# Performance work log

Hardware: AMD Instinct MI355X
Metric: run time of the kernel (lower is better)

Reference implementation:

```python
import jax, jax.numpy as jnp
import numpy as np

D_MODEL = 1024
N_HEADS = 16
HEAD_DIM = D_MODEL // N_HEADS
SEQ = 2048
BATCH = 2
ROPE_BASE = 10000.0


def rope_cos_sin(seq_len, dim, dtype=jnp.float32):
    inv_freq = 1.0 / (ROPE_BASE ** (jnp.arange(0, dim, 2, dtype=jnp.float32) / dim))
    pos = jnp.arange(seq_len, dtype=jnp.float32)
    freqs = jnp.outer(pos, inv_freq)              # [S, dim/2]
    emb = jnp.concatenate([freqs, freqs], axis=-1)  # [S, dim]
    return jnp.cos(emb).astype(dtype), jnp.sin(emb).astype(dtype)


def rotate_half(x):
    x1, x2 = jnp.split(x, 2, axis=-1)
    return jnp.concatenate([-x2, x1], axis=-1)


def setup_inputs() -> dict:
    key = jax.random.key(0)
    kx, kq, kk, kv, ko = jax.random.split(key, 5)
    x = jax.random.normal(kx, (BATCH, SEQ, D_MODEL), dtype=jnp.float32)
    # causal boolean mask, broadcastable to [B, H, S, S]
    attn_mask = jnp.tril(jnp.ones((SEQ, SEQ), dtype=bool))[None, None]
    s = 1.0 / np.sqrt(D_MODEL)
    Wq = jax.random.normal(kq, (D_MODEL, D_MODEL), dtype=jnp.float32) * s
    Wk = jax.random.normal(kk, (D_MODEL, D_MODEL), dtype=jnp.float32) * s
    Wv = jax.random.normal(kv, (D_MODEL, D_MODEL), dtype=jnp.float32) * s
    Wo = jax.random.normal(ko, (D_MODEL, D_MODEL), dtype=jnp.float32) * s
    return {"x": x, "attn_mask": attn_mask, "Wq": Wq, "Wk": Wk, "Wv": Wv, "Wo": Wo}


def reference(x, attn_mask, Wq, Wk, Wv, Wo):
    B, S, _ = x.shape
    dtype = x.dtype
    # projections (nn.Linear: x @ W.T)
    def split_heads(t):
        return t.reshape(B, S, N_HEADS, HEAD_DIM).transpose(0, 2, 1, 3)  # [B,H,S,Dh]
    q = split_heads(x @ Wq.T)
    k = split_heads(x @ Wk.T)
    v = split_heads(x @ Wv.T)
    # RoPE
    cos, sin = rope_cos_sin(S, HEAD_DIM, dtype)  # [S, Dh]
    cos = cos[None, None]
    sin = sin[None, None]
    q = q * cos + rotate_half(q) * sin
    k = k * cos + rotate_half(k) * sin
    # float mask: 0 where True, finfo.min where False
    neg = jnp.finfo(dtype).min
    float_mask = jnp.where(attn_mask, jnp.zeros((), dtype), jnp.full((), neg, dtype))
    # scaled dot product attention
    scale = 1.0 / np.sqrt(HEAD_DIM)
    scores = jnp.einsum("bhqd,bhkd->bhqk", q, k) * scale + float_mask
    attn = jax.nn.softmax(scores, axis=-1)
    out = jnp.einsum("bhqk,bhkd->bhqd", attn, v)  # [B,H,S,Dh]
    out = out.transpose(0, 2, 1, 3).reshape(B, S, D_MODEL)
    return out @ Wo.T
```

## Files before the change

### kernel.cpp

```cpp
#include <hip/hip_runtime.h>
#include <hip/hip_bf16.h>
#include <math.h>

typedef unsigned short ushort_t;
typedef __attribute__((ext_vector_type(8))) short short8;
typedef __attribute__((ext_vector_type(4))) float f32x4;

#define D_MODEL 1024
#define SEQ     2048
#define NH      16
#define HD      64
#define BATCH   2
#define M_TOTAL (BATCH * SEQ)
#define SCL     0.18033688f
#define HSZ     4194304

__device__ __forceinline__ ushort_t f2bf(float f) {
    __hip_bfloat16 h = __float2bfloat16(f);
    ushort_t u;
    __builtin_memcpy(&u, &h, 2);
    return u;
}
__device__ __forceinline__ unsigned pack2(float a, float b) {
    __hip_bfloat162 h = __float22bfloat162_rn(make_float2(a, b));
    unsigned u;
    __builtin_memcpy(&u, &h, 4);
    return u;
}
__device__ __forceinline__ float fexp2(float x) { return __builtin_amdgcn_exp2f(x); }

typedef const __attribute__((address_space(1))) void* gp_t;
typedef __attribute__((address_space(3))) void* lp_t;
__device__ __forceinline__ void cp16(const void* g, void* l) {
    __builtin_amdgcn_global_load_lds((gp_t)g, (lp_t)l, 16, 0, 0);
}

__global__ __launch_bounds__(256) void cvt_bf16(
    const float* __restrict__ x,
    const float* __restrict__ w0, const float* __restrict__ w1,
    const float* __restrict__ w2, const float* __restrict__ w3,
    ushort_t* __restrict__ xb, ushort_t* __restrict__ wb)
{
    size_t e = ((size_t)blockIdx.x * 256 + threadIdx.x) * 8;
    const float* src;
    ushort_t* dst;
    size_t off;
    if (e < (size_t)HSZ) {
        src = x; dst = xb; off = e;
    } else {
        size_t r = e - HSZ;
        int j = (int)(r >> 20);
        off = r & 1048575u;
        src = (j == 0) ? w0 : (j == 1) ? w1 : (j == 2) ? w2 : w3;
        dst = wb + ((size_t)j << 20);
    }
    float4 a = *(const float4*)&src[off];
    float4 b = *(const float4*)&src[off + 4];
    uint4 u;
    u.x = pack2(a.x, a.y);
    u.y = pack2(a.z, a.w);
    u.z = pack2(b.x, b.y);
    u.w = pack2(b.z, b.w);
    *(uint4*)&dst[off] = u;
}

__global__ __launch_bounds__(256) void rope_tab(float2* __restrict__ tab) {
    int idx = blockIdx.x * 256 + threadIdx.x;
    int i = idx & 31, s = idx >> 5;
    float invf = powf(10000.0f, -(float)(2 * i) * (1.0f / 64.0f));
    float fr = (float)s * invf;
    float sn, cs;
    sincosf(fr, &sn, &cs);
    tab[idx] = make_float2(cs, sn);
}

template <int OMODE>
__global__ __launch_bounds__(256) void gemm_k(
    const ushort_t* __restrict__ A,
    const ushort_t* __restrict__ W0, const ushort_t* __restrict__ W1,
    const ushort_t* __restrict__ W2,
    void* __restrict__ D0v, void* __restrict__ D1v, void* __restrict__ D2v,
    const float2* __restrict__ tab)
{
    __shared__ ushort_t As[128 * 32];
    __shared__ ushort_t Bs[128 * 32];
    const int K = D_MODEL;
    const int t = threadIdx.x;
    const int l = t & 63, w = t >> 6;
    const int wm = (w & 1) * 64, wn = (w >> 1) * 64;
    const int r15 = l & 15, q4 = l >> 4;
    const int m0 = blockIdx.y * 128, n0 = blockIdx.x * 128;
    const int z = blockIdx.z;
    const ushort_t* Wp = (z == 0) ? W0 : (z == 1 ? W1 : W2);
    void* Dp           = (z == 0) ? D0v : (z == 1 ? D1v : D2v);

    f32x4 acc[4][4];
#pragma unroll
    for (int i = 0; i < 4; ++i)
#pragma unroll
        for (int j = 0; j < 4; ++j) acc[i][j] = (f32x4){0.f, 0.f, 0.f, 0.f};

    for (int k0 = 0; k0 < K; k0 += 32) {
        __syncthreads();
#pragma unroll
        for (int p = 0; p < 2; ++p) {
            int idx = t + p * 256;
            int row = idx >> 2, kp = (idx & 3) * 8;
            cp16(&A [(size_t)(m0 + row) * K + k0 + kp], &As[idx * 8]);
            cp16(&Wp[(size_t)(n0 + row) * K + k0 + kp], &Bs[idx * 8]);
        }
        __syncthreads();
        short8 af[4], bfr[4];
#pragma unroll
        for (int i = 0; i < 4; ++i)
            af[i] = *(const short8*)&As[(wm + 16 * i + r15) * 32 + q4 * 8];
#pragma unroll
        for (int j = 0; j < 4; ++j)
            bfr[j] = *(const short8*)&Bs[(wn + 16 * j + r15) * 32 + q4 * 8];
#pragma unroll
        for (int i = 0; i < 4; ++i)
#pragma unroll
            for (int j = 0; j < 4; ++j)
                acc[i][j] = __builtin_amdgcn_mfma_f32_16x16x32_bf16(
                    af[i], bfr[j], acc[i][j], 0, 0, 0);
    }

    if (OMODE == 1) {
        float* Dst = (float*)Dp;
#pragma unroll
        for (int i = 0; i < 4; ++i)
#pragma unroll
            for (int j = 0; j < 4; ++j)
#pragma unroll
                for (int r = 0; r < 4; ++r) {
                    int row = m0 + wm + 16 * i + q4 * 4 + r;
                    int col = n0 + wn + 16 * j + r15;
                    Dst[(size_t)row * D_MODEL + col] = acc[i][j][r];
                }
    } else if (z < 2) {
        ushort_t* Dst = (ushort_t*)Dp;
        const float scl = (z == 0) ? SCL : 1.0f;
#pragma unroll
        for (int i = 0; i < 4; ++i) {
#pragma unroll
            for (int r = 0; r < 4; ++r) {
                int row = m0 + wm + 16 * i + q4 * 4 + r;
                int b = row >> 11, s = row & (SEQ - 1);
                const float2* trow = &tab[s * 32];
#pragma unroll
                for (int j = 0; j < 2; ++j) {
                    int col = n0 + wn + 16 * j + r15;
                    int h = col >> 6, f = 16 * j + r15;
                    float2 csn = trow[f];
                    float cs = csn.x * scl, sn = csn.y * scl;
                    float lo = acc[i][j][r], hi = acc[i][j + 2][r];
                    size_t o = (((size_t)(b * NH + h)) * SEQ + s) * HD + f;
                    Dst[o]      = f2bf(lo * cs - hi * sn);
                    Dst[o + 32] = f2bf(hi * cs + lo * sn);
                }
            }
        }
    } else {
        ushort_t* Dst = (ushort_t*)Dp;
#pragma unroll
        for (int i = 0; i < 4; ++i)
#pragma unroll
            for (int j = 0; j < 4; ++j)
#pragma unroll
                for (int r = 0; r < 4; ++r) {
                    int row = m0 + wm + 16 * i + q4 * 4 + r;
                    int col = n0 + wn + 16 * j + r15;
                    int b = row >> 11, s = row & (SEQ - 1);
                    int h = col >> 6, d = col & (HD - 1);
                    size_t o = (((size_t)(b * NH + h)) * HD + d) * SEQ + s;
                    Dst[o] = f2bf(acc[i][j][r]);
                }
    }
}

__global__ __launch_bounds__(256, 3) void attn_fused(
    const ushort_t* __restrict__ Qw, const ushort_t* __restrict__ Kw,
    const ushort_t* __restrict__ Vt, ushort_t* __restrict__ Ow)
{
    __shared__ __align__(16) ushort_t Kl[2][64 * 64];
    __shared__ __align__(16) ushort_t Vl[2][64 * 64];
    __shared__ __align__(16) ushort_t Ps[4][16 * 72];

    const int t = threadIdx.x;
    const int l = t & 63, w = t >> 6;
    const int r15 = l & 15, q4 = l >> 4;
    const int bh = blockIdx.x & 31;
    const int s  = 31 - (int)(blockIdx.x >> 5);
    const int m  = s * 4 + w;
    const size_t baseQK = (size_t)bh * SEQ * HD;
    const size_t baseV  = (size_t)bh * HD * SEQ;

    const int L0 = t, L1 = t + 256;
    const int r0 = L0 >> 3, c0 = (L0 & 7) ^ (r0 & 7);
    const int r1 = L1 >> 3, c1 = (L1 & 7) ^ (r1 & 7);

    const ushort_t* qp = &Qw[baseQK + (size_t)(m * 16 + r15) * HD + q4 * 8];
    short8 qf0 = *(const short8*)qp;
    short8 qf1 = *(const short8*)(qp + 32);

    f32x4 oacc[4];
    float part[4];
#pragma unroll
    for (int nb = 0; nb < 4; ++nb) oacc[nb] = (f32x4){0.f, 0.f, 0.f, 0.f};
#pragma unroll
    for (int r = 0; r < 4; ++r) part[r] = 0.f;

    const int ig0 = m * 16 + q4 * 4;
    ushort_t* ps = &Ps[w][0];

    auto stage = [&](int jt, int buf) {
        cp16(&Kw[baseQK + (size_t)(jt * 64 + r0) * HD + c0 * 8], &Kl[buf][L0 * 8]);
        cp16(&Kw[baseQK + (size_t)(jt * 64 + r1) * HD + c1 * 8], &Kl[buf][L1 * 8]);
        cp16(&Vt[baseV + (size_t)r0 * SEQ + jt * 64 + c0 * 8],   &Vl[buf][L0 * 8]);
        cp16(&Vt[baseV + (size_t)r1 * SEQ + jt * 64 + c1 * 8],   &Vl[buf][L1 * 8]);
    };

    auto process = [&](int jt, int buf) {
        f32x4 sc[4];
#pragma unroll
        for (int nb = 0; nb < 4; ++nb) {
            int R  = nb * 16 + r15;
            int i0 = R * 8 + (q4 ^ (R & 7));
            int i1 = R * 8 + ((q4 + 4) ^ (R & 7));
            short8 kb0 = *(const short8*)&Kl[buf][i0 * 8];
            short8 kb1 = *(const short8*)&Kl[buf][i1 * 8];
            f32x4 zz = (f32x4){0.f, 0.f, 0.f, 0.f};
            zz = __builtin_amdgcn_mfma_f32_16x16x32_bf16(qf0, kb0, zz, 0, 0, 0);
            sc[nb] = __builtin_amdgcn_mfma_f32_16x16x32_bf16(qf1, kb1, zz, 0, 0, 0);
        }
        const bool diag = (jt == s);
#pragma unroll
        for (int r = 0; r < 4; ++r) {
            float p0 = fexp2(sc[0][r]), p1 = fexp2(sc[1][r]);
            float p2 = fexp2(sc[2][r]), p3 = fexp2(sc[3][r]);
            if (diag) {
                int qg = ig0 + r, jb = jt * 64 + r15;
                p0 = (jb      <= qg) ? p0 : 0.f;
                p1 = (jb + 16 <= qg) ? p1 : 0.f;
                p2 = (jb + 32 <= qg) ? p2 : 0.f;
                p3 = (jb + 48 <= qg) ? p3 : 0.f;
            }
            part[r] += (p0 + p1) + (p2 + p3);
            int ro = (q4 * 4 + r) * 72 + r15;
            ps[ro]      = f2bf(p0);
            ps[ro + 16] = f2bf(p1);
            ps[ro + 32] = f2bf(p2);
            ps[ro + 48] = f2bf(p3);
        }
        short8 pf0 = *(const short8*)&ps[r15 * 72 + q4 * 8];
        short8 pf1 = *(const short8*)&ps[r15 * 72 + q4 * 8 + 32];
#pragma unroll
        for (int nb = 0; nb < 4; ++nb) {
            int R  = nb * 16 + r15;
            int i0 = R * 8 + (q4 ^ (R & 7));
            int i1 = R * 8 + ((q4 + 4) ^ (R & 7));
            short8 vb0 = *(const short8*)&Vl[buf][i0 * 8];
            short8 vb1 = *(const short8*)&Vl[buf][i1 * 8];
            f32x4 o = __builtin_amdgcn_mfma_f32_16x16x32_bf16(pf0, vb0, oacc[nb], 0, 0, 0);
            oacc[nb] = __builtin_amdgcn_mfma_f32_16x16x32_bf16(pf1, vb1, o, 0, 0, 0);
        }
    };

    stage(0, 0);
    for (int jt = 0; jt <= s; ++jt) {
        __syncthreads();
        if (jt < s) stage(jt + 1, (jt + 1) & 1);
        process(jt, jt & 1);
    }

    float lsum[4];
#pragma unroll
    for (int r = 0; r < 4; ++r) {
        float rs = part[r];
#pragma unroll
        for (int off = 1; off < 16; off <<= 1)
            rs += __shfl_xor(rs, off, 64);
        lsum[r] = 1.0f / rs;
    }

    const int b = bh >> 4, h = bh & 15;
#pragma unroll
    for (int nb = 0; nb < 4; ++nb) {
#pragma unroll
        for (int r = 0; r < 4; ++r) {
            int sg = m * 16 + q4 * 4 + r;
            int d  = nb * 16 + r15;
            Ow[((size_t)(b * SEQ + sg)) * D_MODEL + h * HD + d] =
                f2bf(oacc[nb][r] * lsum[r]);
        }
    }
}

extern "C" void kernel_launch(void* const* d_in, const int* in_sizes, int n_in,
                              void* d_out, int out_size, void* d_ws, size_t ws_size,
                              hipStream_t stream)
{
    const float* x  = (const float*)d_in[0];
    const float* Wq = (const float*)d_in[2];
    const float* Wk = (const float*)d_in[3];
    const float* Wv = (const float*)d_in[4];
    const float* Wo = (const float*)d_in[5];

    ushort_t* qw = (ushort_t*)d_ws;
    ushort_t* kw = qw + HSZ;
    ushort_t* vt = kw + HSZ;
    ushort_t* xb = vt + HSZ;
    ushort_t* aw = xb;
    ushort_t* wb = xb + HSZ;
    float2*  tab = (float2*)(wb + HSZ);

    cvt_bf16<<<2 * HSZ / 8 / 256, 256, 0, stream>>>(x, Wq, Wk, Wv, Wo, xb, wb);
    rope_tab<<<SEQ * 32 / 256, 256, 0, stream>>>(tab);
    gemm_k<0><<<dim3(D_MODEL / 128, M_TOTAL / 128, 3), 256, 0, stream>>>(
        xb, wb, wb + (1 << 20), wb + (2 << 20), qw, kw, vt, tab);
    attn_fused<<<dim3((SEQ / 64) * 32), 256, 0, stream>>>(qw, kw, vt, aw);
    gemm_k<1><<<dim3(D_MODEL / 128, M_TOTAL / 128, 1), 256, 0, stream>>>(
        aw, wb + (3 << 20), wb + (3 << 20), wb + (3 << 20),
        (float*)d_out, (float*)d_out, (float*)d_out, nullptr);
}
```

Before: 205.5 us.

## Fuse QKV projections per block, double-buffer GEMM staging, merge prep kernels

The two prep kernels (bf16 conversion and RoPE table) become one launch. The QKV GEMM now computes all three projections in one block, so the A tile is loaded once and shared, with 192 accumulators per thread. Both GEMMs double-buffer LDS and prefetch the next K slice while computing, removing one barrier per iteration. The risks are heavy register pressure (launch_bounds 256,1), lower occupancy, and only 256 blocks for the QKV GEMM instead of 768.

```diff
diff --git a/kernel.cpp b/kernel.cpp
--- a/kernel.cpp
+++ b/kernel.cpp
@@ -35,98 +35,115 @@
     __builtin_amdgcn_global_load_lds((gp_t)g, (lp_t)l, 16, 0, 0);
 }
 
-__global__ __launch_bounds__(256) void cvt_bf16(
+__global__ __launch_bounds__(256) void prep(
     const float* __restrict__ x,
     const float* __restrict__ w0, const float* __restrict__ w1,
     const float* __restrict__ w2, const float* __restrict__ w3,
-    ushort_t* __restrict__ xb, ushort_t* __restrict__ wb)
+    ushort_t* __restrict__ xb, ushort_t* __restrict__ wb,
+    float2* __restrict__ tab)
 {
-    size_t e = ((size_t)blockIdx.x * 256 + threadIdx.x) * 8;
-    const float* src;
-    ushort_t* dst;
-    size_t off;
-    if (e < (size_t)HSZ) {
-        src = x; dst = xb; off = e;
+    int bid = blockIdx.x;
+    if (bid < 4096) {
+        size_t e = ((size_t)bid * 256 + threadIdx.x) * 8;
+        const float* src;
+        ushort_t* dst;
+        size_t off;
+        if (e < (size_t)HSZ) {
+            src = x; dst = xb; off = e;
+        } else {
+            size_t r = e - HSZ;
+            int j = (int)(r >> 20);
+            off = r & 1048575u;
+            src = (j == 0) ? w0 : (j == 1) ? w1 : (j == 2) ? w2 : w3;
+            dst = wb + ((size_t)j << 20);
+        }
+        float4 a = *(const float4*)&src[off];
+        float4 b = *(const float4*)&src[off + 4];
+        uint4 u;
+        u.x = pack2(a.x, a.y);
+        u.y = pack2(a.z, a.w);
+        u.z = pack2(b.x, b.y);
+        u.w = pack2(b.z, b.w);
+        *(uint4*)&dst[off] = u;
     } else {
-        size_t r = e - HSZ;
-        int j = (int)(r >> 20);
-        off = r & 1048575u;
-        src = (j == 0) ? w0 : (j == 1) ? w1 : (j == 2) ? w2 : w3;
-        dst = wb + ((size_t)j << 20);
-    }
-    float4 a = *(const float4*)&src[off];
-    float4 b = *(const float4*)&src[off + 4];
-    uint4 u;
-    u.x = pack2(a.x, a.y);
-    u.y = pack2(a.z, a.w);
-    u.z = pack2(b.x, b.y);
-    u.w = pack2(b.z, b.w);
-    *(uint4*)&dst[off] = u;
-}
-
-__global__ __launch_bounds__(256) void rope_tab(float2* __restrict__ tab) {
-    int idx = blockIdx.x * 256 + threadIdx.x;
-    int i = idx & 31, s = idx >> 5;
-    float invf = powf(10000.0f, -(float)(2 * i) * (1.0f / 64.0f));
-    float fr = (float)s * invf;
-    float sn, cs;
-    sincosf(fr, &sn, &cs);
-    tab[idx] = make_float2(cs, sn);
-}
-
-template <int OMODE>
-__global__ __launch_bounds__(256) void gemm_k(
+        int idx = (bid - 4096) * 256 + threadIdx.x;
+        int i = idx & 31, s = idx >> 5;
+        float invf = powf(10000.0f, -(float)(2 * i) * (1.0f / 64.0f));
+        float fr = (float)s * invf;
+        float sn, cs;
+        sincosf(fr, &sn, &cs);
+        tab[idx] = make_float2(cs, sn);
+    }
+}
+
+template <int NZ, int OMODE>
+__global__ __launch_bounds__(256, 1) void gemm_f(
     const ushort_t* __restrict__ A,
     const ushort_t* __restrict__ W0, const ushort_t* __restrict__ W1,
     const ushort_t* __restrict__ W2,
     void* __restrict__ D0v, void* __restrict__ D1v, void* __restrict__ D2v,
     const float2* __restrict__ tab)
 {
-    __shared__ ushort_t As[128 * 32];
-    __shared__ ushort_t Bs[128 * 32];
+    __shared__ ushort_t As[2][128 * 32];
+    __shared__ ushort_t Bs[2][NZ][128 * 32];
     const int K = D_MODEL;
     const int t = threadIdx.x;
     const int l = t & 63, w = t >> 6;
     const int wm = (w & 1) * 64, wn = (w >> 1) * 64;
     const int r15 = l & 15, q4 = l >> 4;
     const int m0 = blockIdx.y * 128, n0 = blockIdx.x * 128;
-    const int z = blockIdx.z;
-    const ushort_t* Wp = (z == 0) ? W0 : (z == 1 ? W1 : W2);
-    void* Dp           = (z == 0) ? D0v : (z == 1 ? D1v : D2v);
-
-    f32x4 acc[4][4];
-#pragma unroll
-    for (int i = 0; i < 4; ++i)
-#pragma unroll
-        for (int j = 0; j < 4; ++j) acc[i][j] = (f32x4){0.f, 0.f, 0.f, 0.f};
-
-    for (int k0 = 0; k0 < K; k0 += 32) {
+    const ushort_t* Wz[3];
+    Wz[0] = W0;
+    if (NZ > 1) { Wz[1] = W1; Wz[2] = W2; }
+
+    f32x4 acc[NZ][4][4];
+#pragma unroll
+    for (int z = 0; z < NZ; ++z)
+#pragma unroll
+        for (int i = 0; i < 4; ++i)
+#pragma unroll
+            for (int j = 0; j < 4; ++j) acc[z][i][j] = (f32x4){0.f, 0.f, 0.f, 0.f};
+
+    const int i0 = t, i1 = t + 256;
+    const int ro0 = i0 >> 2, kp0 = (i0 & 3) * 8;
+    const int ro1 = i1 >> 2, kp1 = (i1 & 3) * 8;
+
+    auto stage = [&](int k0, int buf) {
+        cp16(&A[(size_t)(m0 + ro0) * K + k0 + kp0], &As[buf][i0 * 8]);
+        cp16(&A[(size_t)(m0 + ro1) * K + k0 + kp1], &As[buf][i1 * 8]);
+#pragma unroll
+        for (int z = 0; z < NZ; ++z) {
+            cp16(&Wz[z][(size_t)(n0 + ro0) * K + k0 + kp0], &Bs[buf][z][i0 * 8]);
+            cp16(&Wz[z][(size_t)(n0 + ro1) * K + k0 + kp1], &Bs[buf][z][i1 * 8]);
+        }
+    };
+
+    stage(0, 0);
+    for (int ki = 0; ki < K / 32; ++ki) {
         __syncthreads();
-#pragma unroll
-        for (int p = 0; p < 2; ++p) {
-            int idx = t + p * 256;
-            int row = idx >> 2, kp = (idx & 3) * 8;
-            cp16(&A [(size_t)(m0 + row) * K + k0 + kp], &As[idx * 8]);
-            cp16(&Wp[(size_t)(n0 + row) * K + k0 + kp], &Bs[idx * 8]);
-        }
-        __syncthreads();
-        short8 af[4], bfr[4];
+        if (ki < K / 32 - 1) stage((ki + 1) * 32, (ki + 1) & 1);
+        const int buf = ki & 1;
+        short8 af[4];
 #pragma unroll
         for (int i = 0; i < 4; ++i)
-            af[i] = *(const short8*)&As[(wm + 16 * i + r15) * 32 + q4 * 8];
-#pragma unroll
-        for (int j = 0; j < 4; ++j)
-            bfr[j] = *(const short8*)&Bs[(wn + 16 * j + r15) * 32 + q4 * 8];
-#pragma unroll
-        for (int i = 0; i < 4; ++i)
+            af[i] = *(const short8*)&As[buf][(wm + 16 * i + r15) * 32 + q4 * 8];
+#pragma unroll
+        for (int z = 0; z < NZ; ++z) {
+            short8 bfr[4];
 #pragma unroll
             for (int j = 0; j < 4; ++j)
-                acc[i][j] = __builtin_amdgcn_mfma_f32_16x16x32_bf16(
-                    af[i], bfr[j], acc[i][j], 0, 0, 0);
+                bfr[j] = *(const short8*)&Bs[buf][z][(wn + 16 * j + r15) * 32 + q4 * 8];
+#pragma unroll
+            for (int i = 0; i < 4; ++i)
+#pragma unroll
+                for (int j = 0; j < 4; ++j)
+                    acc[z][i][j] = __builtin_amdgcn_mfma_f32_16x16x32_bf16(
+                        af[i], bfr[j], acc[z][i][j], 0, 0, 0);
+        }
     }
 
     if (OMODE == 1) {
-        float* Dst = (float*)Dp;
+        float* Dst = (float*)D0v;
 #pragma unroll
         for (int i = 0; i < 4; ++i)
 #pragma unroll
@@ -135,46 +152,52 @@
                 for (int r = 0; r < 4; ++r) {
                     int row = m0 + wm + 16 * i + q4 * 4 + r;
                     int col = n0 + wn + 16 * j + r15;
-                    Dst[(size_t)row * D_MODEL + col] = acc[i][j][r];
+                    Dst[(size_t)row * D_MODEL + col] = acc[0][i][j][r];
                 }
-    } else if (z < 2) {
-        ushort_t* Dst = (ushort_t*)Dp;
-        const float scl = (z == 0) ? SCL : 1.0f;
-#pragma unroll
-        for (int i = 0; i < 4; ++i) {
-#pragma unroll
-            for (int r = 0; r < 4; ++r) {
-                int row = m0 + wm + 16 * i + q4 * 4 + r;
-                int b = row >> 11, s = row & (SEQ - 1);
-                const float2* trow = &tab[s * 32];
-#pragma unroll
-                for (int j = 0; j < 2; ++j) {
-                    int col = n0 + wn + 16 * j + r15;
-                    int h = col >> 6, f = 16 * j + r15;
-                    float2 csn = trow[f];
-                    float cs = csn.x * scl, sn = csn.y * scl;
-                    float lo = acc[i][j][r], hi = acc[i][j + 2][r];
-                    size_t o = (((size_t)(b * NH + h)) * SEQ + s) * HD + f;
-                    Dst[o]      = f2bf(lo * cs - hi * sn);
-                    Dst[o + 32] = f2bf(hi * cs + lo * sn);
+    } else {
+#pragma unroll
+        for (int z = 0; z < NZ; ++z) {
+            void* Dp = (z == 0) ? D0v : (z == 1 ? D1v : D2v);
+            if (z < 2) {
+                ushort_t* Dst = (ushort_t*)Dp;
+                const float scl = (z == 0) ? SCL : 1.0f;
+#pragma unroll
+                for (int i = 0; i < 4; ++i) {
+#pragma unroll
+                    for (int r = 0; r < 4; ++r) {
+                        int row = m0 + wm + 16 * i + q4 * 4 + r;
+                        int b = row >> 11, s = row & (SEQ - 1);
+                        const float2* trow = &tab[s * 32];
+#pragma unroll
+                        for (int j = 0; j < 2; ++j) {
+                            int col = n0 + wn + 16 * j + r15;
+                            int h = col >> 6, f = 16 * j + r15;
+                            float2 csn = trow[f];
+                            float cs = csn.x * scl, sn = csn.y * scl;
+                            float lo = acc[z][i][j][r], hi = acc[z][i][j + 2][r];
+                            size_t o = (((size_t)(b * NH + h)) * SEQ + s) * HD + f;
+                            Dst[o]      = f2bf(lo * cs - hi * sn);
+                            Dst[o + 32] = f2bf(hi * cs + lo * sn);
+                        }
+                    }
                 }
+            } else {
+                ushort_t* Dst = (ushort_t*)Dp;
+#pragma unroll
+                for (int i = 0; i < 4; ++i)
+#pragma unroll
+                    for (int j = 0; j < 4; ++j)
+#pragma unroll
+                        for (int r = 0; r < 4; ++r) {
+                            int row = m0 + wm + 16 * i + q4 * 4 + r;
+                            int col = n0 + wn + 16 * j + r15;
+                            int b = row >> 11, s = row & (SEQ - 1);
+                            int h = col >> 6, d = col & (HD - 1);
+                            size_t o = (((size_t)(b * NH + h)) * HD + d) * SEQ + s;
+                            Dst[o] = f2bf(acc[z][i][j][r]);
+                        }
             }
         }
-    } else {
-        ushort_t* Dst = (ushort_t*)Dp;
-#pragma unroll
-        for (int i = 0; i < 4; ++i)
-#pragma unroll
-            for (int j = 0; j < 4; ++j)
-#pragma unroll
-                for (int r = 0; r < 4; ++r) {
-                    int row = m0 + wm + 16 * i + q4 * 4 + r;
-                    int col = n0 + wn + 16 * j + r15;
-                    int b = row >> 11, s = row & (SEQ - 1);
-                    int h = col >> 6, d = col & (HD - 1);
-                    size_t o = (((size_t)(b * NH + h)) * HD + d) * SEQ + s;
-                    Dst[o] = f2bf(acc[i][j][r]);
-                }
     }
 }
 
@@ -225,10 +248,10 @@
 #pragma unroll
         for (int nb = 0; nb < 4; ++nb) {
             int R  = nb * 16 + r15;
-            int i0 = R * 8 + (q4 ^ (R & 7));
-            int i1 = R * 8 + ((q4 + 4) ^ (R & 7));
-            short8 kb0 = *(const short8*)&Kl[buf][i0 * 8];
-            short8 kb1 = *(const short8*)&Kl[buf][i1 * 8];
+            int a0 = R * 8 + (q4 ^ (R & 7));
+            int a1 = R * 8 + ((q4 + 4) ^ (R & 7));
+            short8 kb0 = *(const short8*)&Kl[buf][a0 * 8];
+            short8 kb1 = *(const short8*)&Kl[buf][a1 * 8];
             f32x4 zz = (f32x4){0.f, 0.f, 0.f, 0.f};
             zz = __builtin_amdgcn_mfma_f32_16x16x32_bf16(qf0, kb0, zz, 0, 0, 0);
             sc[nb] = __builtin_amdgcn_mfma_f32_16x16x32_bf16(qf1, kb1, zz, 0, 0, 0);
@@ -257,10 +280,10 @@
 #pragma unroll
         for (int nb = 0; nb < 4; ++nb) {
             int R  = nb * 16 + r15;
-            int i0 = R * 8 + (q4 ^ (R & 7));
-            int i1 = R * 8 + ((q4 + 4) ^ (R & 7));
-            short8 vb0 = *(const short8*)&Vl[buf][i0 * 8];
-            short8 vb1 = *(const short8*)&Vl[buf][i1 * 8];
+            int a0 = R * 8 + (q4 ^ (R & 7));
+            int a1 = R * 8 + ((q4 + 4) ^ (R & 7));
+            short8 vb0 = *(const short8*)&Vl[buf][a0 * 8];
+            short8 vb1 = *(const short8*)&Vl[buf][a1 * 8];
             f32x4 o = __builtin_amdgcn_mfma_f32_16x16x32_bf16(pf0, vb0, oacc[nb], 0, 0, 0);
             oacc[nb] = __builtin_amdgcn_mfma_f32_16x16x32_bf16(pf1, vb1, o, 0, 0, 0);
         }
@@ -314,12 +337,11 @@
     ushort_t* wb = xb + HSZ;
     float2*  tab = (float2*)(wb + HSZ);
 
-    cvt_bf16<<<2 * HSZ / 8 / 256, 256, 0, stream>>>(x, Wq, Wk, Wv, Wo, xb, wb);
-    rope_tab<<<SEQ * 32 / 256, 256, 0, stream>>>(tab);
-    gemm_k<0><<<dim3(D_MODEL / 128, M_TOTAL / 128, 3), 256, 0, stream>>>(
+    prep<<<4096 + 256, 256, 0, stream>>>(x, Wq, Wk, Wv, Wo, xb, wb, tab);
+    gemm_f<3, 0><<<dim3(D_MODEL / 128, M_TOTAL / 128), 256, 0, stream>>>(
         xb, wb, wb + (1 << 20), wb + (2 << 20), qw, kw, vt, tab);
     attn_fused<<<dim3((SEQ / 64) * 32), 256, 0, stream>>>(qw, kw, vt, aw);
-    gemm_k<1><<<dim3(D_MODEL / 128, M_TOTAL / 128, 1), 256, 0, stream>>>(
-        aw, wb + (3 << 20), wb + (3 << 20), wb + (3 << 20),
-        (float*)d_out, (float*)d_out, (float*)d_out, nullptr);
-}
+    gemm_f<1, 1><<<dim3(D_MODEL / 128, M_TOTAL / 128), 256, 0, stream>>>(
+        aw, wb + (3 << 20), nullptr, nullptr,
+        (float*)d_out, nullptr, nullptr, nullptr);
+}
```

After: 217.7 us. 1.06x slower.

## Double GEMM K-tile to 64 with XOR-swizzled LDS and merge prep kernels

Applied to the files above, without the earlier changes.

The projection GEMMs now stage a K-slice of 64 per iteration instead of 32. LDS rows are XOR-swizzled so the wider 128-byte rows do not cause bank conflicts, and this halves the number of barrier pairs per tile. The bf16 conversion and RoPE table kernels are merged into one launch to save a kernel launch. LDS use doubles to 32KB per block, which may reduce occupancy.

```diff
diff --git a/kernel.cpp b/kernel.cpp
--- a/kernel.cpp
+++ b/kernel.cpp
@@ -35,43 +35,45 @@
     __builtin_amdgcn_global_load_lds((gp_t)g, (lp_t)l, 16, 0, 0);
 }
 
-__global__ __launch_bounds__(256) void cvt_bf16(
+__global__ __launch_bounds__(256) void prep(
     const float* __restrict__ x,
     const float* __restrict__ w0, const float* __restrict__ w1,
     const float* __restrict__ w2, const float* __restrict__ w3,
-    ushort_t* __restrict__ xb, ushort_t* __restrict__ wb)
+    ushort_t* __restrict__ xb, ushort_t* __restrict__ wb,
+    float2* __restrict__ tab)
 {
-    size_t e = ((size_t)blockIdx.x * 256 + threadIdx.x) * 8;
-    const float* src;
-    ushort_t* dst;
-    size_t off;
-    if (e < (size_t)HSZ) {
-        src = x; dst = xb; off = e;
+    int bid = blockIdx.x;
+    if (bid < 4096) {
+        size_t e = ((size_t)bid * 256 + threadIdx.x) * 8;
+        const float* src;
+        ushort_t* dst;
+        size_t off;
+        if (e < (size_t)HSZ) {
+            src = x; dst = xb; off = e;
+        } else {
+            size_t r = e - HSZ;
+            int j = (int)(r >> 20);
+            off = r & 1048575u;
+            src = (j == 0) ? w0 : (j == 1) ? w1 : (j == 2) ? w2 : w3;
+            dst = wb + ((size_t)j << 20);
+        }
+        float4 a = *(const float4*)&src[off];
+        float4 b = *(const float4*)&src[off + 4];
+        uint4 u;
+        u.x = pack2(a.x, a.y);
+        u.y = pack2(a.z, a.w);
+        u.z = pack2(b.x, b.y);
+        u.w = pack2(b.z, b.w);
+        *(uint4*)&dst[off] = u;
     } else {
-        size_t r = e - HSZ;
-        int j = (int)(r >> 20);
-        off = r & 1048575u;
-        src = (j == 0) ? w0 : (j == 1) ? w1 : (j == 2) ? w2 : w3;
-        dst = wb + ((size_t)j << 20);
-    }
-    float4 a = *(const float4*)&src[off];
-    float4 b = *(const float4*)&src[off + 4];
-    uint4 u;
-    u.x = pack2(a.x, a.y);
-    u.y = pack2(a.z, a.w);
-    u.z = pack2(b.x, b.y);
-    u.w = pack2(b.z, b.w);
-    *(uint4*)&dst[off] = u;
-}
-
-__global__ __launch_bounds__(256) void rope_tab(float2* __restrict__ tab) {
-    int idx = blockIdx.x * 256 + threadIdx.x;
-    int i = idx & 31, s = idx >> 5;
-    float invf = powf(10000.0f, -(float)(2 * i) * (1.0f / 64.0f));
-    float fr = (float)s * invf;
-    float sn, cs;
-    sincosf(fr, &sn, &cs);
-    tab[idx] = make_float2(cs, sn);
+        int idx = (bid - 4096) * 256 + threadIdx.x;
+        int i = idx & 31, s = idx >> 5;
+        float invf = powf(10000.0f, -(float)(2 * i) * (1.0f / 64.0f));
+        float fr = (float)s * invf;
+        float sn, cs;
+        sincosf(fr, &sn, &cs);
+        tab[idx] = make_float2(cs, sn);
+    }
 }
 
 template <int OMODE>
@@ -82,8 +84,8 @@
     void* __restrict__ D0v, void* __restrict__ D1v, void* __restrict__ D2v,
     const float2* __restrict__ tab)
 {
-    __shared__ ushort_t As[128 * 32];
-    __shared__ ushort_t Bs[128 * 32];
+    __shared__ ushort_t As[128 * 64];
+    __shared__ ushort_t Bs[128 * 64];
     const int K = D_MODEL;
     const int t = threadIdx.x;
     const int l = t & 63, w = t >> 6;
@@ -100,29 +102,37 @@
 #pragma unroll
         for (int j = 0; j < 4; ++j) acc[i][j] = (f32x4){0.f, 0.f, 0.f, 0.f};
 
-    for (int k0 = 0; k0 < K; k0 += 32) {
+    for (int k0 = 0; k0 < K; k0 += 64) {
         __syncthreads();
 #pragma unroll
-        for (int p = 0; p < 2; ++p) {
+        for (int p = 0; p < 4; ++p) {
             int idx = t + p * 256;
-            int row = idx >> 2, kp = (idx & 3) * 8;
-            cp16(&A [(size_t)(m0 + row) * K + k0 + kp], &As[idx * 8]);
-            cp16(&Wp[(size_t)(n0 + row) * K + k0 + kp], &Bs[idx * 8]);
+            int row = idx >> 3, c = idx & 7;
+            int cs = c ^ (row & 7);
+            cp16(&A [(size_t)(m0 + row) * K + k0 + cs * 8], &As[idx * 8]);
+            cp16(&Wp[(size_t)(n0 + row) * K + k0 + cs * 8], &Bs[idx * 8]);
         }
         __syncthreads();
-        short8 af[4], bfr[4];
-#pragma unroll
-        for (int i = 0; i < 4; ++i)
-            af[i] = *(const short8*)&As[(wm + 16 * i + r15) * 32 + q4 * 8];
-#pragma unroll
-        for (int j = 0; j < 4; ++j)
-            bfr[j] = *(const short8*)&Bs[(wn + 16 * j + r15) * 32 + q4 * 8];
-#pragma unroll
-        for (int i = 0; i < 4; ++i)
-#pragma unroll
-            for (int j = 0; j < 4; ++j)
-                acc[i][j] = __builtin_amdgcn_mfma_f32_16x16x32_bf16(
-                    af[i], bfr[j], acc[i][j], 0, 0, 0);
+#pragma unroll
+        for (int kk = 0; kk < 2; ++kk) {
+            short8 af[4], bfr[4];
+#pragma unroll
+            for (int i = 0; i < 4; ++i) {
+                int R = wm + 16 * i + r15;
+                af[i] = *(const short8*)&As[R * 64 + (((kk * 4) + q4 ^ (R & 7))) * 8];
+            }
+#pragma unroll
+            for (int j = 0; j < 4; ++j) {
+                int R = wn + 16 * j + r15;
+                bfr[j] = *(const short8*)&Bs[R * 64 + (((kk * 4) + q4 ^ (R & 7))) * 8];
+            }
+#pragma unroll
+            for (int i = 0; i < 4; ++i)
+#pragma unroll
+                for (int j = 0; j < 4; ++j)
+                    acc[i][j] = __builtin_amdgcn_mfma_f32_16x16x32_bf16(
+                        af[i], bfr[j], acc[i][j], 0, 0, 0);
+        }
     }
 
     if (OMODE == 1) {
@@ -225,10 +235,10 @@
 #pragma unroll
         for (int nb = 0; nb < 4; ++nb) {
             int R  = nb * 16 + r15;
-            int i0 = R * 8 + (q4 ^ (R & 7));
-            int i1 = R * 8 + ((q4 + 4) ^ (R & 7));
-            short8 kb0 = *(const short8*)&Kl[buf][i0 * 8];
-            short8 kb1 = *(const short8*)&Kl[buf][i1 * 8];
+            int a0 = R * 8 + (q4 ^ (R & 7));
+            int a1 = R * 8 + ((q4 + 4) ^ (R & 7));
+            short8 kb0 = *(const short8*)&Kl[buf][a0 * 8];
+            short8 kb1 = *(const short8*)&Kl[buf][a1 * 8];
             f32x4 zz = (f32x4){0.f, 0.f, 0.f, 0.f};
             zz = __builtin_amdgcn_mfma_f32_16x16x32_bf16(qf0, kb0, zz, 0, 0, 0);
             sc[nb] = __builtin_amdgcn_mfma_f32_16x16x32_bf16(qf1, kb1, zz, 0, 0, 0);
@@ -257,10 +267,10 @@
 #pragma unroll
         for (int nb = 0; nb < 4; ++nb) {
             int R  = nb * 16 + r15;
-            int i0 = R * 8 + (q4 ^ (R & 7));
-            int i1 = R * 8 + ((q4 + 4) ^ (R & 7));
-            short8 vb0 = *(const short8*)&Vl[buf][i0 * 8];
-            short8 vb1 = *(const short8*)&Vl[buf][i1 * 8];
+            int a0 = R * 8 + (q4 ^ (R & 7));
+            int a1 = R * 8 + ((q4 + 4) ^ (R & 7));
+            short8 vb0 = *(const short8*)&Vl[buf][a0 * 8];
+            short8 vb1 = *(const short8*)&Vl[buf][a1 * 8];
             f32x4 o = __builtin_amdgcn_mfma_f32_16x16x32_bf16(pf0, vb0, oacc[nb], 0, 0, 0);
             oacc[nb] = __builtin_amdgcn_mfma_f32_16x16x32_bf16(pf1, vb1, o, 0, 0, 0);
         }
@@ -314,12 +324,11 @@
     ushort_t* wb = xb + HSZ;
     float2*  tab = (float2*)(wb + HSZ);
 
-    cvt_bf16<<<2 * HSZ / 8 / 256, 256, 0, stream>>>(x, Wq, Wk, Wv, Wo, xb, wb);
-    rope_tab<<<SEQ * 32 / 256, 256, 0, stream>>>(tab);
+    prep<<<4096 + 256, 256, 0, stream>>>(x, Wq, Wk, Wv, Wo, xb, wb, tab);
     gemm_k<0><<<dim3(D_MODEL / 128, M_TOTAL / 128, 3), 256, 0, stream>>>(
         xb, wb, wb + (1 << 20), wb + (2 << 20), qw, kw, vt, tab);
     attn_fused<<<dim3((SEQ / 64) * 32), 256, 0, stream>>>(qw, kw, vt, aw);
     gemm_k<1><<<dim3(D_MODEL / 128, M_TOTAL / 128, 1), 256, 0, stream>>>(
-        aw, wb + (3 << 20), wb + (3 << 20), wb + (3 << 20),
-        (float*)d_out, (float*)d_out, (float*)d_out, nullptr);
-}
+        aw, wb + (3 << 20), nullptr, nullptr,
+        (float*)d_out, nullptr, nullptr, nullptr);
+}
```

Result: faster. 199.8 us (-2.8%).
